# Kernel optimization log

Measured on AMD Instinct MI355X. Metric: run time of the kernel, lower is better.

The kernel has to match this reference:

```python
import jax, jax.numpy as jnp
import numpy as np

N_HEAD = 12
N_EMBD = 768


def setup_inputs() -> dict:
    key = jax.random.key(0)
    ks = jax.random.split(key, 5)
    B, T, C = 8, 1024, N_EMBD
    x = jax.random.normal(ks[0], (B, T, C), dtype=jnp.float32)
    # c_attn: Linear(C, 3C); c_proj: Linear(C, C). PyTorch Linear: y = x @ W.T + b
    s = 1.0 / np.sqrt(C)
    W_attn = jax.random.uniform(ks[1], (3 * C, C), minval=-s, maxval=s, dtype=jnp.float32)
    b_attn = jax.random.uniform(ks[2], (3 * C,), minval=-s, maxval=s, dtype=jnp.float32)
    W_proj = jax.random.uniform(ks[3], (C, C), minval=-s, maxval=s, dtype=jnp.float32)
    b_proj = jax.random.uniform(ks[4], (C,), minval=-s, maxval=s, dtype=jnp.float32)
    return {"x": x, "W_attn": W_attn, "b_attn": b_attn, "W_proj": W_proj, "b_proj": b_proj}


def reference(x, W_attn, b_attn, W_proj, b_proj):
    B, T, C = x.shape
    H = N_HEAD
    hs = C // H  # head size
    qkv = x @ W_attn.T + b_attn  # [B, T, 3C]
    q, k, v = jnp.split(qkv, 3, axis=2)
    # [B, T, H, hs] -> [B, H, T, hs]
    q = q.reshape(B, T, H, hs).transpose(0, 2, 1, 3)
    k = k.reshape(B, T, H, hs).transpose(0, 2, 1, 3)
    v = v.reshape(B, T, H, hs).transpose(0, 2, 1, 3)
    att = jnp.einsum('bhqd,bhkd->bhqk', q, k) * (1.0 / np.sqrt(hs))
    causal = jnp.tril(jnp.ones((T, T), dtype=bool))
    att = jnp.where(causal, att, -jnp.inf)
    att = jax.nn.softmax(att, axis=-1)
    y = jnp.einsum('bhqk,bhkd->bhqd', att, v)  # [B, H, T, hs]
    y = y.transpose(0, 2, 1, 3).reshape(B, T, C)
    return y @ W_proj.T + b_proj
```

## Files before the change

kernel.cpp:

```cpp
#include <hip/hip_runtime.h>

typedef unsigned short u16;
typedef unsigned int u32;
typedef unsigned long long u64;
typedef __attribute__((ext_vector_type(8))) __bf16 bf16x8;
typedef __attribute__((ext_vector_type(4))) float f32x4;
typedef __attribute__((ext_vector_type(4))) int i32x4;

#define MFMA16(a, b, c) __builtin_amdgcn_mfma_f32_16x16x32_bf16(a, b, c, 0, 0, 0)

__device__ __forceinline__ u16 f2b(float f) {
  __bf16 h = (__bf16)f;
  return __builtin_bit_cast(u16, h);
}

__device__ __forceinline__ void gl_lds16(const void* g, void* l) {
  __builtin_amdgcn_global_load_lds(
      (const __attribute__((address_space(1))) void*)g,
      (__attribute__((address_space(3))) void*)l, 16, 0, 0);
}

__device__ __forceinline__ bf16x8 ldf(const void* p) {
  return __builtin_bit_cast(bf16x8, *(const i32x4*)p);
}

__global__ __launch_bounds__(256) void cvt3_kernel(
    const float4* __restrict__ a, ushort4* __restrict__ oa, int na4,
    const float4* __restrict__ b, ushort4* __restrict__ ob, int nb4,
    const float4* __restrict__ c, ushort4* __restrict__ oc, int nc4) {
  const int step = gridDim.x * blockDim.x;
  const int t0 = blockIdx.x * blockDim.x + threadIdx.x;
  for (int i = t0; i < na4; i += step) {
    float4 v = a[i];
    ushort4 o; o.x = f2b(v.x); o.y = f2b(v.y); o.z = f2b(v.z); o.w = f2b(v.w);
    oa[i] = o;
  }
  for (int i = t0; i < nb4; i += step) {
    float4 v = b[i];
    ushort4 o; o.x = f2b(v.x); o.y = f2b(v.y); o.z = f2b(v.z); o.w = f2b(v.w);
    ob[i] = o;
  }
  for (int i = t0; i < nc4; i += step) {
    float4 v = c[i];
    ushort4 o; o.x = f2b(v.x); o.y = f2b(v.y); o.z = f2b(v.z); o.w = f2b(v.w);
    oc[i] = o;
  }
}

template <int BM, int EPI>
__global__ __launch_bounds__(256, 3) void gemm4(
    const u16* __restrict__ A, const u16* __restrict__ B,
    const float* __restrict__ bias, int M, int N, int K,
    u16* __restrict__ q_s, u16* __restrict__ k_s, u16* __restrict__ vt_s,
    float* __restrict__ outf) {
  constexpr int BN = 192;
  constexpr int MR = BM / 32;
  constexpr int NR = 6;
  constexpr int IA = BM / 32;
  constexpr int IB = 6;
  __shared__ __align__(16) u16 As[BM * 64];
  __shared__ __align__(16) u16 Bs[BN * 64];
  const int tid = threadIdx.x;
  const int w = tid >> 6, l = tid & 63;
  const int lo = l & 15, hi = l >> 4;
  const int wr = w >> 1, wc = w & 1;
  const int nwg = gridDim.x * gridDim.y;
  int bid = blockIdx.y * gridDim.x + blockIdx.x;
  bid = (bid & 7) * (nwg >> 3) + (bid >> 3);
  const int bm0 = (bid / gridDim.x) * BM;
  const int bn0 = (bid % gridDim.x) * BN;
  const size_t Kb = (size_t)K * 2;
  const char* Ab = (const char*)A;
  const char* Bb = (const char*)B;
  const int lrow8 = l >> 3;
  const int lcol = (l & 7) * 16;

  f32x4 acc[MR][NR] = {};

  for (int kt = 0; kt < K; kt += 64) {
    __syncthreads();
#pragma unroll
    for (int i = 0; i < IA; ++i) {
      int rl = (w * IA + i) * 8 + lrow8;
      int cb = lcol ^ ((rl & 7) << 4);
      gl_lds16(Ab + (size_t)(bm0 + rl) * Kb + kt * 2 + cb,
               (char*)As + (w * IA + i) * 1024);
    }
#pragma unroll
    for (int i = 0; i < IB; ++i) {
      int rl = (w * IB + i) * 8 + lrow8;
      int cb = lcol ^ ((rl & 7) << 4);
      gl_lds16(Bb + (size_t)(bn0 + rl) * Kb + kt * 2 + cb,
               (char*)Bs + (w * IB + i) * 1024);
    }
    __syncthreads();
#pragma unroll
    for (int ks = 0; ks < 2; ++ks) {
      bf16x8 bfr[NR];
#pragma unroll
      for (int nf = 0; nf < NR; ++nf) {
        int r = wc * 96 + nf * 16 + lo;
        bfr[nf] = ldf((char*)Bs + r * 128 + ((ks * 64 + hi * 16) ^ ((r & 7) << 4)));
      }
#pragma unroll
      for (int mf = 0; mf < MR; ++mf) {
        int r = wr * (MR * 16) + mf * 16 + lo;
        bf16x8 afr = ldf((char*)As + r * 128 + ((ks * 64 + hi * 16) ^ ((r & 7) << 4)));
#pragma unroll
        for (int nf = 0; nf < NR; ++nf) acc[mf][nf] = MFMA16(afr, bfr[nf], acc[mf][nf]);
      }
    }
  }

#pragma unroll
  for (int nf = 0; nf < NR; ++nf) {
    int col = bn0 + wc * 96 + nf * 16 + lo;
    float bv = bias[col];
    if (EPI == 0) {
      int seg = col / 768;
      int cs = col - seg * 768;
      int h = cs >> 6, d = cs & 63;
      u16* dst = (seg == 0) ? q_s : k_s;
#pragma unroll
      for (int mf = 0; mf < MR; ++mf) {
        int m0 = bm0 + wr * (MR * 16) + mf * 16 + hi * 4;
        int bb = m0 >> 10, t0 = m0 & 1023;
        size_t bh = (size_t)(bb * 12 + h);
        if (seg < 2) {
#pragma unroll
          for (int r = 0; r < 4; ++r)
            dst[(bh * 1024 + t0 + r) * 64 + d] = f2b(acc[mf][nf][r] + bv);
        } else {
          ushort4 pk;
          pk.x = f2b(acc[mf][nf][0] + bv);
          pk.y = f2b(acc[mf][nf][1] + bv);
          pk.z = f2b(acc[mf][nf][2] + bv);
          pk.w = f2b(acc[mf][nf][3] + bv);
          *(ushort4*)&vt_s[(bh * 64 + d) * 1024 + t0] = pk;
        }
      }
    } else {
#pragma unroll
      for (int mf = 0; mf < MR; ++mf) {
        int m0 = bm0 + wr * (MR * 16) + mf * 16 + hi * 4;
#pragma unroll
        for (int r = 0; r < 4; ++r) outf[(size_t)(m0 + r) * N + col] = acc[mf][nf][r] + bv;
      }
    }
  }
}

__global__ __launch_bounds__(256) void attn_kernel(
    const u16* __restrict__ Q, const u16* __restrict__ Kg,
    const u16* __restrict__ Vt, u16* __restrict__ Y) {
  __shared__ __align__(16) u16 Ks[2][64 * 64];
  __shared__ __align__(16) u16 Vs[2][64 * 64];
  __shared__ __align__(16) u16 Ps[4][16 * 64];
  const int tid = threadIdx.x;
  const int w = tid >> 6, l = tid & 63;
  const int lo = l & 15, hi = l >> 4;
  int bid = blockIdx.y * gridDim.x + blockIdx.x;
  bid = (bid & 7) * 96 + (bid >> 3);
  const int bh = bid >> 3;
  const int pr = bid & 7;
  const int b = bh / 12, h = bh % 12;
  const float c1 = 0.125f * 1.44269504f;
  char* pw = (char*)&Ps[w][0];
  const int swl = (lo & 7) << 4;
  const u16* Qb = Q + (size_t)bh * 65536;
  const char* Kbp = (const char*)(Kg + (size_t)bh * 65536);
  const char* Vbp = (const char*)(Vt + (size_t)bh * 65536);

  bf16x8 onesv;
#pragma unroll
  for (int j = 0; j < 8; ++j) onesv[j] = (__bf16)1.0f;

  auto STAGE = [&](int buf, int kb) {
#pragma unroll
    for (int i = 0; i < 2; ++i) {
      int c = w * 2 + i;
      int row = c * 8 + (l >> 3);
      int cb = ((l & 7) * 16) ^ ((row & 7) << 4);
      gl_lds16(Kbp + (size_t)(kb + row) * 128 + cb, (char*)&Ks[buf][0] + c * 1024);
      gl_lds16(Vbp + (size_t)row * 2048 + (size_t)kb * 2 + cb, (char*)&Vs[buf][0] + c * 1024);
    }
  };

  for (int sg = 0; sg < 2; ++sg) {
    const int tile = sg ? (15 - pr) : pr;
    const int q0 = tile * 64 + w * 16;
    const int nt = tile + 1;
    const int qr = q0 + lo;

    bf16x8 qf[2];
#pragma unroll
    for (int ks = 0; ks < 2; ++ks)
      qf[ks] = ldf(Qb + (size_t)(q0 + lo) * 64 + ks * 32 + hi * 8);

    f32x4 o[4] = {};
    f32x4 lsum = {0.f, 0.f, 0.f, 0.f};
    float mrow = -1e30f;

    STAGE(0, 0);
    for (int kt = 0; kt < nt; ++kt) {
      const int cur = kt & 1;
      if (kt + 1 < nt) {
        STAGE(cur ^ 1, (kt + 1) * 64);
        asm volatile("s_waitcnt vmcnt(4)" ::: "memory");
      } else {
        asm volatile("s_waitcnt vmcnt(0)" ::: "memory");
      }
      __builtin_amdgcn_s_barrier();
      __builtin_amdgcn_sched_barrier(0);
      const char* Kt = (const char*)&Ks[cur][0];
      const char* Vv = (const char*)&Vs[cur][0];
      const int kb = kt * 64;

      f32x4 st[4] = {};
      __builtin_amdgcn_s_setprio(1);
#pragma unroll
      for (int kf = 0; kf < 4; ++kf) {
        int rb = (kf * 16 + lo) * 128;
#pragma unroll
        for (int ks = 0; ks < 2; ++ks)
          st[kf] = MFMA16(ldf(Kt + rb + ((ks * 64 + hi * 16) ^ swl)), qf[ks], st[kf]);
      }
      __builtin_amdgcn_s_setprio(0);
      bf16x8 vb[4][2];
#pragma unroll
      for (int nd = 0; nd < 4; ++nd) {
        int rb = (nd * 16 + lo) * 128;
#pragma unroll
        for (int ks = 0; ks < 2; ++ks)
          vb[nd][ks] = ldf(Vv + rb + ((ks * 64 + hi * 16) ^ swl));
      }
      if (kt == nt - 1) {
#pragma unroll
        for (int kf = 0; kf < 4; ++kf)
#pragma unroll
          for (int r = 0; r < 4; ++r) {
            int kcol = kb + kf * 16 + hi * 4 + r;
            if (kcol > qr) st[kf][r] = -1e30f;
          }
      }
      float lm = st[0][0];
#pragma unroll
      for (int kf = 0; kf < 4; ++kf)
#pragma unroll
        for (int r = 0; r < 4; ++r) lm = fmaxf(lm, st[kf][r]);
      if (__any(lm * c1 > mrow + 8.0f)) {
        float LM = fmaxf(lm, __shfl_xor(lm, 16));
        LM = fmaxf(LM, __shfl_xor(LM, 32));
        float Mn = fmaxf(mrow, LM * c1);
        float alP = __builtin_amdgcn_exp2f(mrow - Mn);
        mrow = Mn;
        f32x4 alo;
#pragma unroll
        for (int r = 0; r < 4; ++r) alo[r] = __shfl(alP, hi * 4 + r);
#pragma unroll
        for (int nd = 0; nd < 4; ++nd)
#pragma unroll
          for (int r = 0; r < 4; ++r) o[nd][r] *= alo[r];
#pragma unroll
        for (int r = 0; r < 4; ++r) lsum[r] *= alo[r];
      }
#pragma unroll
      for (int kf = 0; kf < 4; ++kf)
#pragma unroll
        for (int r = 0; r < 4; ++r)
          st[kf][r] = __builtin_amdgcn_exp2f(fmaf(st[kf][r], c1, -mrow));
#pragma unroll
      for (int kf = 0; kf < 4; ++kf) {
        u32 w0 = (u32)f2b(st[kf][0]) | ((u32)f2b(st[kf][1]) << 16);
        u32 w1 = (u32)f2b(st[kf][2]) | ((u32)f2b(st[kf][3]) << 16);
        *(u64*)(pw + lo * 128 + ((kf * 32 + hi * 8) ^ swl)) =
            (u64)w0 | ((u64)w1 << 32);
      }
      bf16x8 pa[2];
#pragma unroll
      for (int ks = 0; ks < 2; ++ks)
        pa[ks] = ldf(pw + lo * 128 + ((ks * 64 + hi * 16) ^ swl));
      __builtin_amdgcn_s_setprio(1);
#pragma unroll
      for (int ks = 0; ks < 2; ++ks) {
#pragma unroll
        for (int nd = 0; nd < 4; ++nd) o[nd] = MFMA16(pa[ks], vb[nd][ks], o[nd]);
        lsum = MFMA16(pa[ks], onesv, lsum);
      }
      __builtin_amdgcn_s_setprio(0);
      __builtin_amdgcn_sched_barrier(0);
      __builtin_amdgcn_s_barrier();
    }

    f32x4 inv;
#pragma unroll
    for (int r = 0; r < 4; ++r) inv[r] = 1.0f / lsum[r];
#pragma unroll
    for (int nd = 0; nd < 4; ++nd)
#pragma unroll
      for (int r = 0; r < 4; ++r) {
        int t = q0 + hi * 4 + r;
        int d = nd * 16 + lo;
        Y[((size_t)b * 1024 + t) * 768 + h * 64 + d] = f2b(o[nd][r] * inv[r]);
      }
  }
}

extern "C" void kernel_launch(void* const* d_in, const int* in_sizes, int n_in,
                              void* d_out, int out_size, void* d_ws, size_t ws_size,
                              hipStream_t stream) {
  const float* x  = (const float*)d_in[0];
  const float* Wa = (const float*)d_in[1];
  const float* ba = (const float*)d_in[2];
  const float* Wp = (const float*)d_in[3];
  const float* bp = (const float*)d_in[4];
  float* out = (float*)d_out;
  char* ws = (char*)d_ws;

  constexpr size_t XB  = 0;
  constexpr size_t WAB = 12582912;
  constexpr size_t WPB = WAB + 3538944;
  constexpr size_t QS  = WPB + 1179648;
  constexpr size_t KS  = QS + 12582912;
  constexpr size_t VTS = KS + 12582912;
  constexpr size_t YB  = VTS + 12582912;

  u16* xb  = (u16*)(ws + XB);
  u16* wab = (u16*)(ws + WAB);
  u16* wpb = (u16*)(ws + WPB);
  u16* qs  = (u16*)(ws + QS);
  u16* ks  = (u16*)(ws + KS);
  u16* vts = (u16*)(ws + VTS);
  u16* yb  = (u16*)(ws + YB);

  cvt3_kernel<<<2048, 256, 0, stream>>>(
      (const float4*)x,  (ushort4*)xb,  8192 * 768 / 4,
      (const float4*)Wa, (ushort4*)wab, 2304 * 768 / 4,
      (const float4*)Wp, (ushort4*)wpb, 768 * 768 / 4);

  gemm4<128, 0><<<dim3(12, 64), 256, 0, stream>>>(xb, wab, ba, 8192, 2304, 768,
                                                  qs, ks, vts, nullptr);
  attn_kernel<<<dim3(8, 96), 256, 0, stream>>>(qs, ks, vts, yb);
  gemm4<64, 1><<<dim3(4, 128), 256, 0, stream>>>(yb, wpb, bp, 8192, 768, 768,
                                                 nullptr, nullptr, nullptr, out);
}
```

Baseline: 96.44 us.

## Process paired causal query tiles together sharing each staged K/V tile

The attention kernel used to run its two query tiles (pr and 15-pr) one after the other, staging K/V separately for each. It now processes both tiles in a single loop over the longer tile's key blocks, so every staged K/V tile is reused by both query tiles while the shorter tile is active. This roughly halves K/V global loads and barriers per block. In exchange it doubles the accumulator registers and adds a launch-bounds occupancy hint and a tree-style max reduction. There is a risk of register pressure or spills, and the P scratch buffer in LDS is reused by both tiles within one iteration.

```diff
diff --git a/kernel.cpp b/kernel.cpp
--- a/kernel.cpp
+++ b/kernel.cpp
@@ -12,6 +12,10 @@
 __device__ __forceinline__ u16 f2b(float f) {
   __bf16 h = (__bf16)f;
   return __builtin_bit_cast(u16, h);
+}
+
+__device__ __forceinline__ float mx3(float a, float b, float c) {
+  return fmaxf(fmaxf(a, b), c);
 }
 
 __device__ __forceinline__ void gl_lds16(const void* g, void* l) {
@@ -150,7 +154,7 @@
   }
 }
 
-__global__ __launch_bounds__(256) void attn_kernel(
+__global__ __launch_bounds__(256, 3) void attn_kernel(
     const u16* __restrict__ Q, const u16* __restrict__ Kg,
     const u16* __restrict__ Vt, u16* __restrict__ Y) {
   __shared__ __align__(16) u16 Ks[2][64 * 64];
@@ -186,95 +190,109 @@
     }
   };
 
-  for (int sg = 0; sg < 2; ++sg) {
-    const int tile = sg ? (15 - pr) : pr;
-    const int q0 = tile * 64 + w * 16;
-    const int nt = tile + 1;
-    const int qr = q0 + lo;
-
-    bf16x8 qf[2];
-#pragma unroll
-    for (int ks = 0; ks < 2; ++ks)
-      qf[ks] = ldf(Qb + (size_t)(q0 + lo) * 64 + ks * 32 + hi * 8);
-
-    f32x4 o[4] = {};
-    f32x4 lsum = {0.f, 0.f, 0.f, 0.f};
-    float mrow = -1e30f;
-
-    STAGE(0, 0);
-    for (int kt = 0; kt < nt; ++kt) {
-      const int cur = kt & 1;
-      if (kt + 1 < nt) {
-        STAGE(cur ^ 1, (kt + 1) * 64);
-        asm volatile("s_waitcnt vmcnt(4)" ::: "memory");
-      } else {
-        asm volatile("s_waitcnt vmcnt(0)" ::: "memory");
-      }
-      __builtin_amdgcn_s_barrier();
-      __builtin_amdgcn_sched_barrier(0);
-      const char* Kt = (const char*)&Ks[cur][0];
-      const char* Vv = (const char*)&Vs[cur][0];
-      const int kb = kt * 64;
-
-      f32x4 st[4] = {};
-      __builtin_amdgcn_s_setprio(1);
-#pragma unroll
-      for (int kf = 0; kf < 4; ++kf) {
-        int rb = (kf * 16 + lo) * 128;
-#pragma unroll
-        for (int ks = 0; ks < 2; ++ks)
-          st[kf] = MFMA16(ldf(Kt + rb + ((ks * 64 + hi * 16) ^ swl)), qf[ks], st[kf]);
-      }
-      __builtin_amdgcn_s_setprio(0);
-      bf16x8 vb[4][2];
-#pragma unroll
-      for (int nd = 0; nd < 4; ++nd) {
-        int rb = (nd * 16 + lo) * 128;
-#pragma unroll
-        for (int ks = 0; ks < 2; ++ks)
-          vb[nd][ks] = ldf(Vv + rb + ((ks * 64 + hi * 16) ^ swl));
-      }
-      if (kt == nt - 1) {
-#pragma unroll
-        for (int kf = 0; kf < 4; ++kf)
-#pragma unroll
-          for (int r = 0; r < 4; ++r) {
-            int kcol = kb + kf * 16 + hi * 4 + r;
-            if (kcol > qr) st[kf][r] = -1e30f;
-          }
-      }
-      float lm = st[0][0];
+  const int q0A = pr * 64 + w * 16;
+  const int q0B = (15 - pr) * 64 + w * 16;
+  const int ntA = pr + 1;
+  const int nt = 16 - pr;
+  const int qrA = q0A + lo;
+  const int qrB = q0B + lo;
+
+  bf16x8 qfA[2], qfB[2];
+#pragma unroll
+  for (int ks = 0; ks < 2; ++ks) {
+    qfA[ks] = ldf(Qb + (size_t)(q0A + lo) * 64 + ks * 32 + hi * 8);
+    qfB[ks] = ldf(Qb + (size_t)(q0B + lo) * 64 + ks * 32 + hi * 8);
+  }
+
+  f32x4 oA[4] = {}, oB[4] = {};
+  f32x4 lsA = {0.f, 0.f, 0.f, 0.f}, lsB = {0.f, 0.f, 0.f, 0.f};
+  float mA = -1e30f, mB = -1e30f;
+
+  STAGE(0, 0);
+  for (int kt = 0; kt < nt; ++kt) {
+    const int cur = kt & 1;
+    if (kt + 1 < nt) {
+      STAGE(cur ^ 1, (kt + 1) * 64);
+      asm volatile("s_waitcnt vmcnt(4)" ::: "memory");
+    } else {
+      asm volatile("s_waitcnt vmcnt(0)" ::: "memory");
+    }
+    __builtin_amdgcn_s_barrier();
+    __builtin_amdgcn_sched_barrier(0);
+    const char* Kt = (const char*)&Ks[cur][0];
+    const char* Vv = (const char*)&Vs[cur][0];
+    const int kb = kt * 64;
+    const bool actA = kt < ntA;
+
+    f32x4 sA[4] = {}, sB[4] = {};
+    __builtin_amdgcn_s_setprio(1);
+#pragma unroll
+    for (int kf = 0; kf < 4; ++kf) {
+      int rb = (kf * 16 + lo) * 128;
+#pragma unroll
+      for (int ks = 0; ks < 2; ++ks) {
+        bf16x8 kk = ldf(Kt + rb + ((ks * 64 + hi * 16) ^ swl));
+        sB[kf] = MFMA16(kk, qfB[ks], sB[kf]);
+        if (actA) sA[kf] = MFMA16(kk, qfA[ks], sA[kf]);
+      }
+    }
+    __builtin_amdgcn_s_setprio(0);
+    bf16x8 vb[4][2];
+#pragma unroll
+    for (int nd = 0; nd < 4; ++nd) {
+      int rb = (nd * 16 + lo) * 128;
+#pragma unroll
+      for (int ks = 0; ks < 2; ++ks)
+        vb[nd][ks] = ldf(Vv + rb + ((ks * 64 + hi * 16) ^ swl));
+    }
+    if (kt == nt - 1) {
 #pragma unroll
       for (int kf = 0; kf < 4; ++kf)
 #pragma unroll
-        for (int r = 0; r < 4; ++r) lm = fmaxf(lm, st[kf][r]);
-      if (__any(lm * c1 > mrow + 8.0f)) {
+        for (int r = 0; r < 4; ++r)
+          if (kb + kf * 16 + hi * 4 + r > qrB) sB[kf][r] = -1e30f;
+    }
+    if (actA && kt == ntA - 1) {
+#pragma unroll
+      for (int kf = 0; kf < 4; ++kf)
+#pragma unroll
+        for (int r = 0; r < 4; ++r)
+          if (kb + kf * 16 + hi * 4 + r > qrA) sA[kf][r] = -1e30f;
+    }
+
+    {
+      float t0 = mx3(sB[0][0], sB[0][1], sB[0][2]);
+      float t1 = mx3(sB[0][3], sB[1][0], sB[1][1]);
+      float t2 = mx3(sB[1][2], sB[1][3], sB[2][0]);
+      float t3 = mx3(sB[2][1], sB[2][2], sB[2][3]);
+      float t4 = mx3(sB[3][0], sB[3][1], sB[3][2]);
+      float lm = fmaxf(mx3(t0, t1, t2), mx3(t3, t4, sB[3][3]));
+      if (__any(lm * c1 > mB + 8.0f)) {
         float LM = fmaxf(lm, __shfl_xor(lm, 16));
         LM = fmaxf(LM, __shfl_xor(LM, 32));
-        float Mn = fmaxf(mrow, LM * c1);
-        float alP = __builtin_amdgcn_exp2f(mrow - Mn);
-        mrow = Mn;
+        float Mn = fmaxf(mB, LM * c1);
+        float alP = __builtin_amdgcn_exp2f(mB - Mn);
+        mB = Mn;
         f32x4 alo;
 #pragma unroll
         for (int r = 0; r < 4; ++r) alo[r] = __shfl(alP, hi * 4 + r);
 #pragma unroll
         for (int nd = 0; nd < 4; ++nd)
 #pragma unroll
-          for (int r = 0; r < 4; ++r) o[nd][r] *= alo[r];
-#pragma unroll
-        for (int r = 0; r < 4; ++r) lsum[r] *= alo[r];
+          for (int r = 0; r < 4; ++r) oB[nd][r] *= alo[r];
+#pragma unroll
+        for (int r = 0; r < 4; ++r) lsB[r] *= alo[r];
       }
 #pragma unroll
       for (int kf = 0; kf < 4; ++kf)
 #pragma unroll
         for (int r = 0; r < 4; ++r)
-          st[kf][r] = __builtin_amdgcn_exp2f(fmaf(st[kf][r], c1, -mrow));
+          sB[kf][r] = __builtin_amdgcn_exp2f(fmaf(sB[kf][r], c1, -mB));
 #pragma unroll
       for (int kf = 0; kf < 4; ++kf) {
-        u32 w0 = (u32)f2b(st[kf][0]) | ((u32)f2b(st[kf][1]) << 16);
-        u32 w1 = (u32)f2b(st[kf][2]) | ((u32)f2b(st[kf][3]) << 16);
-        *(u64*)(pw + lo * 128 + ((kf * 32 + hi * 8) ^ swl)) =
-            (u64)w0 | ((u64)w1 << 32);
+        u32 w0 = (u32)f2b(sB[kf][0]) | ((u32)f2b(sB[kf][1]) << 16);
+        u32 w1 = (u32)f2b(sB[kf][2]) | ((u32)f2b(sB[kf][3]) << 16);
+        *(u64*)(pw + lo * 128 + ((kf * 32 + hi * 8) ^ swl)) = (u64)w0 | ((u64)w1 << 32);
       }
       bf16x8 pa[2];
 #pragma unroll
@@ -284,17 +302,72 @@
 #pragma unroll
       for (int ks = 0; ks < 2; ++ks) {
 #pragma unroll
-        for (int nd = 0; nd < 4; ++nd) o[nd] = MFMA16(pa[ks], vb[nd][ks], o[nd]);
-        lsum = MFMA16(pa[ks], onesv, lsum);
+        for (int nd = 0; nd < 4; ++nd) oB[nd] = MFMA16(pa[ks], vb[nd][ks], oB[nd]);
+        lsB = MFMA16(pa[ks], onesv, lsB);
       }
       __builtin_amdgcn_s_setprio(0);
-      __builtin_amdgcn_sched_barrier(0);
-      __builtin_amdgcn_s_barrier();
-    }
-
+    }
+
+    if (actA) {
+      float t0 = mx3(sA[0][0], sA[0][1], sA[0][2]);
+      float t1 = mx3(sA[0][3], sA[1][0], sA[1][1]);
+      float t2 = mx3(sA[1][2], sA[1][3], sA[2][0]);
+      float t3 = mx3(sA[2][1], sA[2][2], sA[2][3]);
+      float t4 = mx3(sA[3][0], sA[3][1], sA[3][2]);
+      float lm = fmaxf(mx3(t0, t1, t2), mx3(t3, t4, sA[3][3]));
+      if (__any(lm * c1 > mA + 8.0f)) {
+        float LM = fmaxf(lm, __shfl_xor(lm, 16));
+        LM = fmaxf(LM, __shfl_xor(LM, 32));
+        float Mn = fmaxf(mA, LM * c1);
+        float alP = __builtin_amdgcn_exp2f(mA - Mn);
+        mA = Mn;
+        f32x4 alo;
+#pragma unroll
+        for (int r = 0; r < 4; ++r) alo[r] = __shfl(alP, hi * 4 + r);
+#pragma unroll
+        for (int nd = 0; nd < 4; ++nd)
+#pragma unroll
+          for (int r = 0; r < 4; ++r) oA[nd][r] *= alo[r];
+#pragma unroll
+        for (int r = 0; r < 4; ++r) lsA[r] *= alo[r];
+      }
+#pragma unroll
+      for (int kf = 0; kf < 4; ++kf)
+#pragma unroll
+        for (int r = 0; r < 4; ++r)
+          sA[kf][r] = __builtin_amdgcn_exp2f(fmaf(sA[kf][r], c1, -mA));
+#pragma unroll
+      for (int kf = 0; kf < 4; ++kf) {
+        u32 w0 = (u32)f2b(sA[kf][0]) | ((u32)f2b(sA[kf][1]) << 16);
+        u32 w1 = (u32)f2b(sA[kf][2]) | ((u32)f2b(sA[kf][3]) << 16);
+        *(u64*)(pw + lo * 128 + ((kf * 32 + hi * 8) ^ swl)) = (u64)w0 | ((u64)w1 << 32);
+      }
+      bf16x8 pa[2];
+#pragma unroll
+      for (int ks = 0; ks < 2; ++ks)
+        pa[ks] = ldf(pw + lo * 128 + ((ks * 64 + hi * 16) ^ swl));
+      __builtin_amdgcn_s_setprio(1);
+#pragma unroll
+      for (int ks = 0; ks < 2; ++ks) {
+#pragma unroll
+        for (int nd = 0; nd < 4; ++nd) oA[nd] = MFMA16(pa[ks], vb[nd][ks], oA[nd]);
+        lsA = MFMA16(pa[ks], onesv, lsA);
+      }
+      __builtin_amdgcn_s_setprio(0);
+    }
+
+    __builtin_amdgcn_sched_barrier(0);
+    __builtin_amdgcn_s_barrier();
+  }
+
+#pragma unroll
+  for (int s = 0; s < 2; ++s) {
+    const int q0 = s ? q0B : q0A;
+    f32x4* o = s ? oB : oA;
+    f32x4 ls = s ? lsB : lsA;
     f32x4 inv;
 #pragma unroll
-    for (int r = 0; r < 4; ++r) inv[r] = 1.0f / lsum[r];
+    for (int r = 0; r < 4; ++r) inv[r] = 1.0f / ls[r];
 #pragma unroll
     for (int nd = 0; nd < 4; ++nd)
 #pragma unroll
```

New measurement: 99.69 us. 3.4% more time.
